# Kernel optimization log

Measured on AMD Instinct MI355X. Metric: run time of the kernel, lower is better.

The kernel has to match this reference:

```python
import jax, jax.numpy as jnp
import numpy as np

B, T, D, L, K = 4, 2048, 2048, 2048, 4  # batch, seq, width, lru_width, conv temporal width


def setup_inputs() -> dict:
    key = jax.random.key(0)
    ks = jax.random.split(key, 12)
    s = 0.02
    f32 = jnp.float32
    return {
        "x": jax.random.normal(ks[0], (B, T, D), f32),
        "w_y": jax.random.normal(ks[1], (D, L), f32) * s,
        "b_y": jnp.zeros((L,), f32),
        "w_x": jax.random.normal(ks[2], (D, L), f32) * s,
        "b_x": jnp.zeros((L,), f32),
        "conv_w": jax.random.normal(ks[3], (K, L), f32) * s,
        "conv_b": jnp.zeros((L,), f32),
        "a_param": jax.random.uniform(ks[4], (L,), f32, 0.5, 4.0),
        "w_ig": jax.random.normal(ks[5], (L, L), f32) * s,
        "b_ig": jnp.zeros((L,), f32),
        "w_ag": jax.random.normal(ks[6], (L, L), f32) * s,
        "b_ag": jnp.zeros((L,), f32),
        "w_out": jax.random.normal(ks[7], (L, D), f32) * s,
        "b_out": jnp.zeros((D,), f32),
    }


def reference(x, w_y, b_y, w_x, b_x, conv_w, conv_b, a_param,
              w_ig, b_ig, w_ag, b_ag, w_out, b_out):
    # x: [B, T, D] (batch_first=True)
    Tn = x.shape[1]
    # gate branch: GELU(linear_y(x))
    y = jax.nn.gelu(jnp.einsum('btd,dl->btl', x, w_y) + b_y, approximate=False)
    # recurrent branch: linear_x -> causal depthwise conv1d (width K)
    xb = jnp.einsum('btd,dl->btl', x, w_x) + b_x
    xp = jnp.pad(xb, ((0, 0), (K - 1, 0), (0, 0)))  # zero left pad (fresh cache)
    conv = conv_b
    for k in range(K):  # y_t = b + sum_k w[k] * x_{t-(K-1-k)}
        conv = conv + conv_w[k] * xp[:, k:k + Tn]
    # RG-LRU
    gate_x = jax.nn.sigmoid(jnp.einsum('btl,lm->btm', conv, w_ig) + b_ig)
    gate_a = jax.nn.sigmoid(jnp.einsum('btl,lm->btm', conv, w_ag) + b_ag)
    log_a = -8.0 * gate_a * jax.nn.softplus(a_param)  # [B,T,L]
    a = jnp.exp(log_a)
    mult = jnp.sqrt(1.0 - jnp.exp(2.0 * log_a))
    reset = (jnp.arange(Tn) == 0)[None, :, None]  # reset at sequence start
    a = jnp.where(reset, 0.0, a)
    mult = jnp.where(reset, 1.0, mult)
    nx = gate_x * conv * mult
    # linear diagonal scan h_t = a_t * h_{t-1} + nx_t
    def step(h, inp):
        a_t, x_t = inp
        h = a_t * h + x_t
        return h, h
    h0 = jnp.zeros((x.shape[0], a.shape[-1]), x.dtype)
    hn, hs = jax.lax.scan(step, h0, (a.transpose(1, 0, 2), nx.transpose(1, 0, 2)))
    h_seq = hs.transpose(1, 0, 2)  # [B,T,L]
    out = jnp.einsum('btl,ld->btd', h_seq * y, w_out) + b_out
    return out, hn
```

## Files before the change

kernel.cpp:

```cpp
#include <hip/hip_runtime.h>
#include <math.h>

#define B_ 4
#define T_ 2048
#define D_ 2048
#define L_ 2048
#define KW 4
#define M_ (B_*T_)

typedef unsigned short u16;
typedef unsigned short u16x8 __attribute__((ext_vector_type(8)));
typedef __bf16 bf16x8 __attribute__((ext_vector_type(8)));
typedef float f32x4 __attribute__((ext_vector_type(4)));

__device__ __forceinline__ u16 f2bf(float f) {
    unsigned u = __float_as_uint(f);
    u += 0x7fffu + ((u >> 16) & 1u);
    return (u16)(u >> 16);
}
__device__ __forceinline__ float bf2f(u16 h) {
    return __uint_as_float(((unsigned)h) << 16);
}
__device__ __forceinline__ float gelu_exact(float v) {
    return 0.5f * v * (1.0f + erff(v * 0.70710678118654752440f));
}
__device__ __forceinline__ float sigmoidf_(float v) {
    return 1.0f / (1.0f + __expf(-v));
}
__device__ __forceinline__ void gload16(const void* g, void* l) {
    __builtin_amdgcn_global_load_lds(
        (const __attribute__((address_space(1))) void*)g,
        (__attribute__((address_space(3))) void*)l,
        16, 0, 0);
}
__device__ __forceinline__ void barf() {
    __builtin_amdgcn_sched_barrier(0);
    __builtin_amdgcn_s_barrier();
    __builtin_amdgcn_sched_barrier(0);
}

__global__ __launch_bounds__(256)
void castx_kernel(const float* __restrict__ in, u16* __restrict__ out)
{
    const int i = blockIdx.x * 256 + threadIdx.x;
    float4 v = ((const float4*)in)[i];
    ushort4 o;
    o.x = f2bf(v.x); o.y = f2bf(v.y); o.z = f2bf(v.z); o.w = f2bf(v.w);
    ((ushort4*)out)[i] = o;
}

__global__ __launch_bounds__(256)
void transcast_kernel(const float* __restrict__ in, u16* __restrict__ out,
                      int Kd, int Nd)
{
    __shared__ float tile[32][33];
    const int bx = blockIdx.x;
    const int by = blockIdx.y;
    const int tx = threadIdx.x & 31;
    const int ty = threadIdx.x >> 5;
    #pragma unroll
    for (int j = 0; j < 4; ++j) {
        const int r = by*32 + ty + j*8;
        tile[ty + j*8][tx] = in[(size_t)r * Nd + bx*32 + tx];
    }
    __syncthreads();
    #pragma unroll
    for (int j = 0; j < 4; ++j) {
        const int n = bx*32 + ty + j*8;
        out[(size_t)n * Kd + by*32 + tx] = f2bf(tile[tx][ty + j*8]);
    }
}

__device__ __forceinline__ void store_out(float* C, size_t idx, float v) { C[idx] = v; }
__device__ __forceinline__ void store_out(u16*   C, size_t idx, float v) { C[idx] = f2bf(v); }

template<int EPI, typename OutT>
__global__ __launch_bounds__(512)
void mgemm_kernel(const u16* __restrict__ A, const u16* __restrict__ BT,
                  const float* __restrict__ bias, OutT* __restrict__ C,
                  int M, int N, int K)
{
    __shared__ __align__(16) u16 lds[49152];
    u16* ldsB = lds + 32768;

    const int tid  = threadIdx.x;
    const int wave = tid >> 6;
    const int lane = tid & 63;

    const int nbx = N >> 7;
    const int nwg = nbx * (M >> 8);
    const int bid = blockIdx.x;
    const int li  = (bid & 7) * (nwg >> 3) + (bid >> 3);
    const int bm  = (li / nbx) * 256;
    const int bn  = (li % nbx) * 128;

    const int wm = wave >> 1;
    const int wn = wave & 1;
    const int lr = lane & 15;
    const int q  = lane >> 4;
    const int sw = lane & 7;

    const int grow8 = lane >> 3;
    const int gslot = (lane & 7) ^ grow8;

    const int NT = K >> 6;

    const int cA0 = (wave >> 1) * 8 + (wave & 1) * 2;
    const int cB0 = (wave >> 2) * 8 + (wave & 3);

    const u16* gA0 = A  + (size_t)(bm + (cA0    )*8 + grow8) * K + gslot*8;
    const u16* gA1 = A  + (size_t)(bm + (cA0 + 1)*8 + grow8) * K + gslot*8;
    const u16* gA2 = A  + (size_t)(bm + (cA0 + 4)*8 + grow8) * K + gslot*8;
    const u16* gA3 = A  + (size_t)(bm + (cA0 + 5)*8 + grow8) * K + gslot*8;
    const u16* gB0 = BT + (size_t)(bn + (cB0    )*8 + grow8) * K + gslot*8;
    const u16* gB1 = BT + (size_t)(bn + (cB0 + 4)*8 + grow8) * K + gslot*8;
    const int dA0 = (cA0    )*512 + lane*8, dA1 = (cA0+1)*512 + lane*8;
    const int dA2 = (cA0 + 4)*512 + lane*8, dA3 = (cA0+5)*512 + lane*8;
    const int dB0 = (cB0    )*512 + lane*8, dB1 = (cB0+4)*512 + lane*8;

    auto ST_AH0 = [&](int g){ u16* b = lds  + (g&1)*16384; const size_t kg = (size_t)g<<6;
        gload16(gA0+kg, &b[dA0]); gload16(gA1+kg, &b[dA1]); };
    auto ST_AH1 = [&](int g){ u16* b = lds  + (g&1)*16384; const size_t kg = (size_t)g<<6;
        gload16(gA2+kg, &b[dA2]); gload16(gA3+kg, &b[dA3]); };
    auto ST_BH0 = [&](int g){ u16* b = ldsB + (g&1)*8192;  const size_t kg = (size_t)g<<6;
        gload16(gB0+kg, &b[dB0]); };
    auto ST_BH1 = [&](int g){ u16* b = ldsB + (g&1)*8192;  const size_t kg = (size_t)g<<6;
        gload16(gB1+kg, &b[dB1]); };

    const int ks0 = ((    q) ^ sw) * 8;
    const int ks1 = ((4 + q) ^ sw) * 8;

    auto LD_AF = [&](const u16* Ab, int half, bf16x8 (&dst)[2][2]) {
        #pragma unroll
        for (int i = 0; i < 2; ++i) {
            const int ro = (wm*64 + half*32 + i*16 + lr) * 64;
            dst[i][0] = *(const bf16x8*)&Ab[ro + ks0];
            dst[i][1] = *(const bf16x8*)&Ab[ro + ks1];
        }
    };
    auto LD_BF = [&](const u16* Bb, int half, bf16x8 (&dst)[2][2]) {
        #pragma unroll
        for (int j = 0; j < 2; ++j) {
            const int ro = (wn*64 + half*32 + j*16 + lr) * 64;
            dst[j][0] = *(const bf16x8*)&Bb[ro + ks0];
            dst[j][1] = *(const bf16x8*)&Bb[ro + ks1];
        }
    };

    f32x4 acc[4][4] = {};
    bf16x8 af0[2][2], af1[2][2], bf0A[2][2], bf0B[2][2], bf1[2][2];

    auto MM = [&](int mh, int nh, bf16x8 (&a)[2][2], bf16x8 (&b)[2][2]) {
        __builtin_amdgcn_s_setprio(1);
        #pragma unroll
        for (int ks = 0; ks < 2; ++ks)
            #pragma unroll
            for (int i = 0; i < 2; ++i)
                #pragma unroll
                for (int j = 0; j < 2; ++j)
                    acc[mh*2+i][nh*2+j] = __builtin_amdgcn_mfma_f32_16x16x32_bf16(
                        a[i][ks], b[j][ks], acc[mh*2+i][nh*2+j], 0, 0, 0);
        __builtin_amdgcn_s_setprio(0);
    };

    ST_AH0(0); ST_BH1(0); ST_AH1(0); ST_BH0(0);
    ST_AH0(1); ST_BH1(1); ST_AH1(1); ST_BH0(1);
    asm volatile("s_waitcnt vmcnt(6)" ::: "memory");
    barf();
    LD_AF(lds, 0, af0);
    LD_BF(ldsB, 0, bf0A);

    auto ktile = [&](int g, bf16x8 (&bfc)[2][2], bf16x8 (&bfn)[2][2]) {
        const u16* Ab = lds  + (g&1)*16384;
        const u16* Bb = ldsB + (g&1)*8192;
        const bool s1 = (g + 1 < NT), s2 = (g + 2 < NT);

        LD_BF(Bb, 1, bf1);
        MM(0, 0, af0, bfc);
        barf();

        LD_AF(Ab, 1, af1);
        if (s2) ST_AH0(g + 2);
        MM(0, 1, af0, bf1);
        barf();

        if (s2) ST_BH1(g + 2);
        MM(1, 1, af1, bf1);
        if (s1) {
            if (s2) { asm volatile("s_waitcnt vmcnt(3)" ::: "memory"); }
            else    { asm volatile("s_waitcnt vmcnt(0)" ::: "memory"); }
        }
        barf();

        if (s1) {
            const u16* AbN = lds  + ((g+1)&1)*16384;
            const u16* BbN = ldsB + ((g+1)&1)*8192;
            LD_AF(AbN, 0, af0);
            LD_BF(BbN, 0, bfn);
            if (s2) { ST_AH1(g + 2); ST_BH0(g + 2); }
        }
        MM(1, 0, af1, bfc);
        barf();
    };

    for (int g = 0; g < NT; g += 2) {
        ktile(g,     bf0A, bf0B);
        ktile(g + 1, bf0B, bf0A);
    }

    const int orow = (lane >> 4) * 4;
    float bv[4];
    #pragma unroll
    for (int nj = 0; nj < 4; ++nj) bv[nj] = bias[bn + wn*64 + nj*16 + lr];
    #pragma unroll
    for (int mi = 0; mi < 4; ++mi) {
        #pragma unroll
        for (int r = 0; r < 4; ++r) {
            const int row = bm + wm*64 + mi*16 + orow + r;
            const size_t rb = (size_t)row * N + bn + wn*64 + lr;
            #pragma unroll
            for (int nj = 0; nj < 4; ++nj) {
                float v = acc[mi][nj][r] + bv[nj];
                if (EPI == 1)      v = gelu_exact(v);
                else if (EPI == 2) v = sigmoidf_(v);
                store_out(C, rb + nj*16, v);
            }
        }
    }
}

__global__ __launch_bounds__(256)
void conv_kernel(const u16* __restrict__ xb, const float* __restrict__ cw,
                 const float* __restrict__ cb, u16* __restrict__ out)
{
    const int idx = blockIdx.x * 256 + threadIdx.x;
    const int NL8 = L_ / 8;
    const int l = (idx % NL8) * 8;
    const int bt = idx / NL8;
    const int t = bt & (T_ - 1);
    float acc[8];
    #pragma unroll
    for (int j = 0; j < 8; ++j) acc[j] = cb[l + j];
    #pragma unroll
    for (int k = 0; k < KW; ++k) {
        const int ts = t - (KW-1) + k;
        if (ts >= 0) {
            u16x8 xv = *(const u16x8*)(xb + ((size_t)(bt - (KW-1-k))) * L_ + l);
            #pragma unroll
            for (int j = 0; j < 8; ++j)
                acc[j] = fmaf(cw[k*L_ + l + j], bf2f(xv[j]), acc[j]);
        }
    }
    u16x8 o;
    #pragma unroll
    for (int j = 0; j < 8; ++j) o[j] = f2bf(acc[j]);
    *(u16x8*)(out + (size_t)bt * L_ + l) = o;
}

__global__ __launch_bounds__(256)
void rglru_kernel(const u16* __restrict__ conv, u16* __restrict__ gxa,
                  u16* __restrict__ ganx, const float* __restrict__ ap)
{
    const int idx = blockIdx.x * 256 + threadIdx.x;
    const int NL8 = L_ / 8;
    const int l = (idx % NL8) * 8;
    const int bt = idx / NL8;
    const int t = bt & (T_ - 1);
    const size_t off = (size_t)bt * L_ + l;
    u16x8 gx = *(u16x8*)(gxa + off);
    u16x8 ga = *(u16x8*)(ganx + off);
    u16x8 cv = *(const u16x8*)(conv + off);
    u16x8 av, nxv;
    #pragma unroll
    for (int j = 0; j < 8; ++j) {
        float p  = ap[l + j];
        float sp = log1pf(expf(p));
        float la = -8.0f * bf2f(ga[j]) * sp;
        float a  = expf(la);
        float mult = sqrtf(fmaxf(0.f, 1.0f - a*a));
        if (t == 0) { a = 0.f; mult = 1.f; }
        av[j]  = f2bf(a);
        nxv[j] = f2bf(bf2f(gx[j]) * bf2f(cv[j]) * mult);
    }
    *(u16x8*)(gxa + off)  = av;
    *(u16x8*)(ganx + off) = nxv;
}

#define CHUNKS 32
#define CLEN (T_ / CHUNKS)

__global__ __launch_bounds__(256)
void scan1_kernel(const u16* __restrict__ Ab, const u16* __restrict__ Xb,
                  float* __restrict__ Pb, float* __restrict__ Sb)
{
    const int l = blockIdx.x * 256 + threadIdx.x;
    const int c = blockIdx.y;
    const int b = blockIdx.z;
    size_t base = ((size_t)b * T_ + (size_t)c * CLEN) * L_ + l;
    float h = 0.f, P = 1.f;
    #pragma unroll 4
    for (int t = 0; t < CLEN; ++t) {
        float a = bf2f(Ab[base + (size_t)t * L_]);
        float x = bf2f(Xb[base + (size_t)t * L_]);
        h = fmaf(a, h, x);
        P *= a;
    }
    const size_t o = ((size_t)b * CHUNKS + c) * L_ + l;
    Pb[o] = P;
    Sb[o] = h;
}

__global__ __launch_bounds__(256)
void scan2_kernel(const float* __restrict__ Pb, const float* __restrict__ Sb,
                  float* __restrict__ Hin, float* __restrict__ hn)
{
    const int idx = blockIdx.x * 256 + threadIdx.x;
    const int l = idx & (L_ - 1);
    const int b = idx >> 11;
    float h = 0.f;
    for (int c = 0; c < CHUNKS; ++c) {
        const size_t o = ((size_t)b * CHUNKS + c) * L_ + l;
        Hin[o] = h;
        h = fmaf(Pb[o], h, Sb[o]);
    }
    hn[(size_t)b * L_ + l] = h;
}

__global__ __launch_bounds__(256)
void scan3_kernel(const u16* __restrict__ Ab, const u16* __restrict__ Xb,
                  const float* __restrict__ Hin, const u16* __restrict__ Yb,
                  u16* __restrict__ Zb)
{
    const int l = blockIdx.x * 256 + threadIdx.x;
    const int c = blockIdx.y;
    const int b = blockIdx.z;
    float h = Hin[((size_t)b * CHUNKS + c) * L_ + l];
    size_t base = ((size_t)b * T_ + (size_t)c * CLEN) * L_ + l;
    #pragma unroll 4
    for (int t = 0; t < CLEN; ++t) {
        const size_t o = base + (size_t)t * L_;
        h = fmaf(bf2f(Ab[o]), h, bf2f(Xb[o]));
        Zb[o] = f2bf(h * bf2f(Yb[o]));
    }
}

extern "C" void kernel_launch(void* const* d_in, const int* in_sizes, int n_in,
                              void* d_out, int out_size, void* d_ws, size_t ws_size,
                              hipStream_t stream)
{
    const float* x     = (const float*)d_in[0];
    const float* w_y   = (const float*)d_in[1];
    const float* b_y   = (const float*)d_in[2];
    const float* w_x   = (const float*)d_in[3];
    const float* b_x   = (const float*)d_in[4];
    const float* cw    = (const float*)d_in[5];
    const float* cb    = (const float*)d_in[6];
    const float* ap    = (const float*)d_in[7];
    const float* w_ig  = (const float*)d_in[8];
    const float* b_ig  = (const float*)d_in[9];
    const float* w_ag  = (const float*)d_in[10];
    const float* b_ag  = (const float*)d_in[11];
    const float* w_out = (const float*)d_in[12];
    const float* b_out = (const float*)d_in[13];

    float* out = (float*)d_out;
    float* hn  = out + (size_t)M_ * D_;

    const size_t MB = 1u << 20;
    char* w = (char*)d_ws;
    u16*  xbf   = (u16*)(w + 0);
    u16*  wigb  = (u16*)(w + 0);
    u16*  wagb  = (u16*)(w + 8*MB);
    u16*  zb    = (u16*)(w + 0);
    u16*  ybf   = (u16*)(w + 32*MB);
    u16*  xbbf  = (u16*)(w + 64*MB);
    u16*  woutb = (u16*)(w + 64*MB);
    float* Pb   = (float*)(w + 72*MB);
    float* Sb   = (float*)(w + 73*MB);
    float* Hin  = (float*)(w + 74*MB);
    u16*  wyb   = (u16*)(w + 96*MB);
    u16*  wxb   = (u16*)(w + 104*MB);
    u16*  convb = (u16*)(w + 96*MB);
    u16*  gx    = (u16*)(w + 128*MB);
    u16*  ga    = (u16*)(w + 160*MB);

    const dim3 blk(256);
    const dim3 blkG(512);
    const dim3 gG((L_/128) * (M_/256));
    const dim3 gT(2048/32, 2048/32);
    const int  gE8 = (M_ * L_ / 8) / 256;
    const dim3 gScan(L_/256, CHUNKS, B_);

    hipLaunchKernelGGL(castx_kernel, dim3((M_*D_/4)/256), blk, 0, stream, x, xbf);
    hipLaunchKernelGGL(transcast_kernel, gT, blk, 0, stream, w_y, wyb, D_, L_);
    hipLaunchKernelGGL(transcast_kernel, gT, blk, 0, stream, w_x, wxb, D_, L_);
    hipLaunchKernelGGL((mgemm_kernel<1, u16>), gG, blkG, 0, stream, xbf, wyb, b_y, ybf, M_, L_, D_);
    hipLaunchKernelGGL((mgemm_kernel<0, u16>), gG, blkG, 0, stream, xbf, wxb, b_x, xbbf, M_, L_, D_);
    hipLaunchKernelGGL(transcast_kernel, gT, blk, 0, stream, w_ig, wigb, L_, L_);
    hipLaunchKernelGGL(transcast_kernel, gT, blk, 0, stream, w_ag, wagb, L_, L_);
    hipLaunchKernelGGL(conv_kernel, dim3(gE8), blk, 0, stream, xbbf, cw, cb, convb);
    hipLaunchKernelGGL(transcast_kernel, gT, blk, 0, stream, w_out, woutb, L_, D_);
    hipLaunchKernelGGL((mgemm_kernel<2, u16>), gG, blkG, 0, stream, convb, wigb, b_ig, gx, M_, L_, L_);
    hipLaunchKernelGGL((mgemm_kernel<2, u16>), gG, blkG, 0, stream, convb, wagb, b_ag, ga, M_, L_, L_);
    hipLaunchKernelGGL(rglru_kernel, dim3(gE8), blk, 0, stream, convb, gx, ga, ap);
    hipLaunchKernelGGL(scan1_kernel, gScan, blk, 0, stream, gx, ga, Pb, Sb);
    hipLaunchKernelGGL(scan2_kernel, dim3(B_*L_/256), blk, 0, stream, Pb, Sb, Hin, hn);
    hipLaunchKernelGGL(scan3_kernel, gScan, blk, 0, stream, gx, ga, Hin, ybf, zb);
    hipLaunchKernelGGL((mgemm_kernel<0, float>), gG, blkG, 0, stream, zb, woutb, b_out, out, M_, D_, L_);
}
```

Baseline: 577.3 us.

## Enlarge GEMM tiles to 256x256 with 8x4 per-wave accumulators

The bf16 MFMA GEMM goes from 256x128 to 256x256 block tiles, with a 2x4 wave grid where each wave computes a 128x64 sub-tile. The goal is more operand reuse per byte loaded from global memory and LDS. The k-loop is rewritten as a simpler single-tile loop that waits on lgkmcnt(0) before each MFMA group instead of software-pipelining fragment loads across k-tiles. The trade-offs are higher register pressure from 32 accumulators, 128KB of LDS, half as many workgroups per GEMM, and more exposed LDS latency.

```diff
diff --git a/kernel.cpp b/kernel.cpp
--- a/kernel.cpp
+++ b/kernel.cpp
@@ -33,7 +33,7 @@
         (__attribute__((address_space(3))) void*)l,
         16, 0, 0);
 }
-__device__ __forceinline__ void barf() {
+__device__ __forceinline__ void pbar() {
     __builtin_amdgcn_sched_barrier(0);
     __builtin_amdgcn_s_barrier();
     __builtin_amdgcn_sched_barrier(0);
@@ -80,22 +80,23 @@
                   const float* __restrict__ bias, OutT* __restrict__ C,
                   int M, int N, int K)
 {
-    __shared__ __align__(16) u16 lds[49152];
+    __shared__ __align__(16) u16 lds[65536];
+    u16* ldsA = lds;
     u16* ldsB = lds + 32768;
 
     const int tid  = threadIdx.x;
     const int wave = tid >> 6;
     const int lane = tid & 63;
 
-    const int nbx = N >> 7;
+    const int nbx = N >> 8;
     const int nwg = nbx * (M >> 8);
     const int bid = blockIdx.x;
     const int li  = (bid & 7) * (nwg >> 3) + (bid >> 3);
     const int bm  = (li / nbx) * 256;
-    const int bn  = (li % nbx) * 128;
-
-    const int wm = wave >> 1;
-    const int wn = wave & 1;
+    const int bn  = (li % nbx) * 256;
+
+    const int wm = wave >> 2;
+    const int wn = wave & 3;
     const int lr = lane & 15;
     const int q  = lane >> 4;
     const int sw = lane & 7;
@@ -105,40 +106,41 @@
 
     const int NT = K >> 6;
 
-    const int cA0 = (wave >> 1) * 8 + (wave & 1) * 2;
-    const int cB0 = (wave >> 2) * 8 + (wave & 3);
-
-    const u16* gA0 = A  + (size_t)(bm + (cA0    )*8 + grow8) * K + gslot*8;
-    const u16* gA1 = A  + (size_t)(bm + (cA0 + 1)*8 + grow8) * K + gslot*8;
-    const u16* gA2 = A  + (size_t)(bm + (cA0 + 4)*8 + grow8) * K + gslot*8;
-    const u16* gA3 = A  + (size_t)(bm + (cA0 + 5)*8 + grow8) * K + gslot*8;
-    const u16* gB0 = BT + (size_t)(bn + (cB0    )*8 + grow8) * K + gslot*8;
-    const u16* gB1 = BT + (size_t)(bn + (cB0 + 4)*8 + grow8) * K + gslot*8;
-    const int dA0 = (cA0    )*512 + lane*8, dA1 = (cA0+1)*512 + lane*8;
-    const int dA2 = (cA0 + 4)*512 + lane*8, dA3 = (cA0+5)*512 + lane*8;
-    const int dB0 = (cB0    )*512 + lane*8, dB1 = (cB0+4)*512 + lane*8;
-
-    auto ST_AH0 = [&](int g){ u16* b = lds  + (g&1)*16384; const size_t kg = (size_t)g<<6;
+    const int c1 = (wave & 3) + (wave >> 2) * 8;
+    const u16* gA0 = A  + (size_t)(bm + (wave     )*8 + grow8) * K + gslot*8;
+    const u16* gA1 = A  + (size_t)(bm + (wave + 16)*8 + grow8) * K + gslot*8;
+    const u16* gA2 = A  + (size_t)(bm + (wave +  8)*8 + grow8) * K + gslot*8;
+    const u16* gA3 = A  + (size_t)(bm + (wave + 24)*8 + grow8) * K + gslot*8;
+    const u16* gB0 = BT + (size_t)(bn + (c1       )*8 + grow8) * K + gslot*8;
+    const u16* gB1 = BT + (size_t)(bn + (c1  + 16 )*8 + grow8) * K + gslot*8;
+    const u16* gB2 = BT + (size_t)(bn + (c1  +  4 )*8 + grow8) * K + gslot*8;
+    const u16* gB3 = BT + (size_t)(bn + (c1  + 20 )*8 + grow8) * K + gslot*8;
+    const int dA0 = (wave     )*512 + lane*8, dA1 = (wave + 16)*512 + lane*8;
+    const int dA2 = (wave +  8)*512 + lane*8, dA3 = (wave + 24)*512 + lane*8;
+    const int dB0 = (c1       )*512 + lane*8, dB1 = (c1  + 16 )*512 + lane*8;
+    const int dB2 = (c1  +  4 )*512 + lane*8, dB3 = (c1  + 20 )*512 + lane*8;
+
+    auto ST_AH0 = [&](int g){ u16* b = ldsA + (g&1)*16384; const size_t kg = (size_t)g<<6;
         gload16(gA0+kg, &b[dA0]); gload16(gA1+kg, &b[dA1]); };
-    auto ST_AH1 = [&](int g){ u16* b = lds  + (g&1)*16384; const size_t kg = (size_t)g<<6;
+    auto ST_AH1 = [&](int g){ u16* b = ldsA + (g&1)*16384; const size_t kg = (size_t)g<<6;
         gload16(gA2+kg, &b[dA2]); gload16(gA3+kg, &b[dA3]); };
-    auto ST_BH0 = [&](int g){ u16* b = ldsB + (g&1)*8192;  const size_t kg = (size_t)g<<6;
-        gload16(gB0+kg, &b[dB0]); };
-    auto ST_BH1 = [&](int g){ u16* b = ldsB + (g&1)*8192;  const size_t kg = (size_t)g<<6;
-        gload16(gB1+kg, &b[dB1]); };
+    auto ST_BH0 = [&](int g){ u16* b = ldsB + (g&1)*16384; const size_t kg = (size_t)g<<6;
+        gload16(gB0+kg, &b[dB0]); gload16(gB1+kg, &b[dB1]); };
+    auto ST_BH1 = [&](int g){ u16* b = ldsB + (g&1)*16384; const size_t kg = (size_t)g<<6;
+        gload16(gB2+kg, &b[dB2]); gload16(gB3+kg, &b[dB3]); };
 
     const int ks0 = ((    q) ^ sw) * 8;
     const int ks1 = ((4 + q) ^ sw) * 8;
 
-    auto LD_AF = [&](const u16* Ab, int half, bf16x8 (&dst)[2][2]) {
+    auto LDA4 = [&](const u16* Ab, int half, bf16x8 (&dst)[4][2]) {
         #pragma unroll
-        for (int i = 0; i < 2; ++i) {
-            const int ro = (wm*64 + half*32 + i*16 + lr) * 64;
+        for (int i = 0; i < 4; ++i) {
+            const int ro = (wm*128 + half*64 + i*16 + lr) * 64;
             dst[i][0] = *(const bf16x8*)&Ab[ro + ks0];
             dst[i][1] = *(const bf16x8*)&Ab[ro + ks1];
         }
     };
-    auto LD_BF = [&](const u16* Bb, int half, bf16x8 (&dst)[2][2]) {
+    auto LDB2 = [&](const u16* Bb, int half, bf16x8 (&dst)[2][2]) {
         #pragma unroll
         for (int j = 0; j < 2; ++j) {
             const int ro = (wn*64 + half*32 + j*16 + lr) * 64;
@@ -147,65 +149,62 @@
         }
     };
 
-    f32x4 acc[4][4] = {};
-    bf16x8 af0[2][2], af1[2][2], bf0A[2][2], bf0B[2][2], bf1[2][2];
-
-    auto MM = [&](int mh, int nh, bf16x8 (&a)[2][2], bf16x8 (&b)[2][2]) {
+    f32x4 acc[8][4] = {};
+    bf16x8 a0[4][2], a1[4][2], b0[2][2], b1[2][2];
+
+    auto MM16 = [&](bf16x8 (&a)[4][2], bf16x8 (&b)[2][2], int mo, int no) {
         __builtin_amdgcn_s_setprio(1);
         #pragma unroll
         for (int ks = 0; ks < 2; ++ks)
             #pragma unroll
-            for (int i = 0; i < 2; ++i)
+            for (int ii = 0; ii < 4; ++ii)
                 #pragma unroll
-                for (int j = 0; j < 2; ++j)
-                    acc[mh*2+i][nh*2+j] = __builtin_amdgcn_mfma_f32_16x16x32_bf16(
-                        a[i][ks], b[j][ks], acc[mh*2+i][nh*2+j], 0, 0, 0);
+                for (int jj = 0; jj < 2; ++jj)
+                    acc[mo+ii][no+jj] = __builtin_amdgcn_mfma_f32_16x16x32_bf16(
+                        a[ii][ks], b[jj][ks], acc[mo+ii][no+jj], 0, 0, 0);
         __builtin_amdgcn_s_setprio(0);
     };
 
-    ST_AH0(0); ST_BH1(0); ST_AH1(0); ST_BH0(0);
-    ST_AH0(1); ST_BH1(1); ST_AH1(1); ST_BH0(1);
-    asm volatile("s_waitcnt vmcnt(6)" ::: "memory");
-    barf();
-    LD_AF(lds, 0, af0);
-    LD_BF(ldsB, 0, bf0A);
-
-    auto ktile = [&](int g, bf16x8 (&bfc)[2][2], bf16x8 (&bfn)[2][2]) {
-        const u16* Ab = lds  + (g&1)*16384;
-        const u16* Bb = ldsB + (g&1)*8192;
+    #define LGKM0() do { asm volatile("s_waitcnt lgkmcnt(0)" ::: "memory"); \
+                         __builtin_amdgcn_sched_barrier(0); } while(0)
+
+    ST_AH0(0); ST_BH0(0); ST_AH1(0); ST_BH1(0);
+    ST_AH0(1); ST_BH0(1); ST_AH1(1); ST_BH1(1);
+    asm volatile("s_waitcnt vmcnt(8)" ::: "memory");
+    pbar();
+
+    for (int g = 0; g < NT; ++g) {
+        const u16* Ab = ldsA + (g&1)*16384;
+        const u16* Bb = ldsB + (g&1)*16384;
         const bool s1 = (g + 1 < NT), s2 = (g + 2 < NT);
 
-        LD_BF(Bb, 1, bf1);
-        MM(0, 0, af0, bfc);
-        barf();
-
-        LD_AF(Ab, 1, af1);
+        LDA4(Ab, 0, a0);
+        LDB2(Bb, 0, b0);
+        pbar();
+        LGKM0();
+        MM16(a0, b0, 0, 0);
+        pbar();
+
+        LDB2(Bb, 1, b1);
         if (s2) ST_AH0(g + 2);
-        MM(0, 1, af0, bf1);
-        barf();
-
-        if (s2) ST_BH1(g + 2);
-        MM(1, 1, af1, bf1);
-        if (s1) {
-            if (s2) { asm volatile("s_waitcnt vmcnt(3)" ::: "memory"); }
-            else    { asm volatile("s_waitcnt vmcnt(0)" ::: "memory"); }
-        }
-        barf();
-
-        if (s1) {
-            const u16* AbN = lds  + ((g+1)&1)*16384;
-            const u16* BbN = ldsB + ((g+1)&1)*8192;
-            LD_AF(AbN, 0, af0);
-            LD_BF(BbN, 0, bfn);
-            if (s2) { ST_AH1(g + 2); ST_BH0(g + 2); }
-        }
-        MM(1, 0, af1, bfc);
-        barf();
-    };
-
-    for (int g = 0; g < NT; g += 2) {
-        ktile(g,     bf0A, bf0B);
-        ktile(g + 1, bf0B, bf0A);
+        pbar();
+        LGKM0();
+        MM16(a0, b1, 0, 2);
+        pbar();
+
+        LDA4(Ab, 1, a1);
+        if (s2) ST_BH0(g + 2);
+        pbar();
+        LGKM0();
+        MM16(a1, b1, 4, 2);
+        pbar();
+
+        if (s2) { ST_AH1(g + 2); ST_BH1(g + 2); }
+        pbar();
+        MM16(a1, b0, 4, 0);
+        if (s2)      { asm volatile("s_waitcnt vmcnt(8)" ::: "memory"); }
+        else if (s1) { asm volatile("s_waitcnt vmcnt(0)" ::: "memory"); }
+        pbar();
     }
 
     const int orow = (lane >> 4) * 4;
@@ -213,10 +212,10 @@
     #pragma unroll
     for (int nj = 0; nj < 4; ++nj) bv[nj] = bias[bn + wn*64 + nj*16 + lr];
     #pragma unroll
-    for (int mi = 0; mi < 4; ++mi) {
+    for (int mi = 0; mi < 8; ++mi) {
         #pragma unroll
         for (int r = 0; r < 4; ++r) {
-            const int row = bm + wm*64 + mi*16 + orow + r;
+            const int row = bm + wm*128 + mi*16 + orow + r;
             const size_t rb = (size_t)row * N + bn + wn*64 + lr;
             #pragma unroll
             for (int nj = 0; nj < 4; ++nj) {
@@ -227,6 +226,7 @@
             }
         }
     }
+    #undef LGKM0
 }
 
 __global__ __launch_bounds__(256)
@@ -386,7 +386,7 @@
 
     const dim3 blk(256);
     const dim3 blkG(512);
-    const dim3 gG((L_/128) * (M_/256));
+    const dim3 gG((L_/256) * (M_/256));
     const dim3 gT(2048/32, 2048/32);
     const int  gE8 = (M_ * L_ / 8) / 256;
     const dim3 gScan(L_/256, CHUNKS, B_);
```

After: 544.8 us. -5.6%, faster.
